# Performance work log

Measured on AMD Instinct MI355X. Metric: run time of the kernel, lower is better.

The kernel has to match this reference:

```python
import jax, jax.numpy as jnp
import numpy as np

B, N, D, C, IN, S = 64, 8192, 64, 256, 128, 3
CTRL_IN = IN + D  # input concatenated with 1 read vector
EPS = 1e-8


def _address(h, mem, prev_w, Wk, bk, Wb, bb, Wg, bg, Ws, bs, Wgam, bgam):
    """NTM content+location addressing. h:[B,C], mem:[B,N,D], prev_w:[B,N] -> [B,N]."""
    k = h @ Wk + bk                                   # [B,D]
    beta = jax.nn.softplus(h @ Wb + bb)               # [B,1]
    g = jax.nn.sigmoid(h @ Wg + bg)                   # [B,1]
    s = jax.nn.softmax(h @ Ws + bs, axis=-1)          # [B,S]
    gamma = jax.nn.softplus(h @ Wgam + bgam) + 1.0    # [B,1]
    # cosine similarity of key vs each memory row
    dots = jnp.einsum('bnd,bd->bn', mem, k)           # [B,N]
    norms = jnp.linalg.norm(mem, axis=-1) * jnp.linalg.norm(k, axis=-1, keepdims=True)
    sim = dots / (norms + EPS)
    wc = jax.nn.softmax(beta * sim, axis=-1)          # content weights
    wg = g * wc + (1.0 - g) * prev_w                  # interpolation gate
    # circular convolution with shift kernel, offsets [-1, 0, 1]
    offsets = [j - S // 2 for j in range(S)]
    ws = sum(s[:, j:j + 1] * jnp.roll(wg, offsets[j], axis=1) for j in range(S))
    # sharpening
    wpow = ws ** gamma
    return wpow / (jnp.sum(wpow, axis=-1, keepdims=True) + EPS)


def setup_inputs() -> dict:
    key = jax.random.key(0)
    ks = jax.random.split(key, 40)

    def p(k, shape):
        return jax.random.normal(k, shape, jnp.float32) / np.sqrt(shape[0]).astype(np.float32)

    inp = {
        'x': jax.random.normal(ks[0], (B, IN), jnp.float32),
        'prev_memory': jax.random.uniform(ks[1], (B, N, D), jnp.float32),
        'prev_read_weights': jax.random.uniform(ks[2], (B, N), jnp.float32),
        'prev_write_weights': jax.random.uniform(ks[3], (B, N), jnp.float32),
        'prev_read_vector': jax.random.normal(ks[4], (B, D), jnp.float32),
        # feedforward controller
        'W_ctrl': p(ks[5], (CTRL_IN, C)), 'b_ctrl': jnp.zeros((C,), jnp.float32),
        # read head
        'Wk_r': p(ks[6], (C, D)), 'bk_r': jnp.zeros((D,), jnp.float32),
        'Wb_r': p(ks[7], (C, 1)), 'bb_r': jnp.zeros((1,), jnp.float32),
        'Wg_r': p(ks[8], (C, 1)), 'bg_r': jnp.zeros((1,), jnp.float32),
        'Ws_r': p(ks[9], (C, S)), 'bs_r': jnp.zeros((S,), jnp.float32),
        'Wgam_r': p(ks[10], (C, 1)), 'bgam_r': jnp.zeros((1,), jnp.float32),
        # write head
        'Wk_w': p(ks[11], (C, D)), 'bk_w': jnp.zeros((D,), jnp.float32),
        'Wb_w': p(ks[12], (C, 1)), 'bb_w': jnp.zeros((1,), jnp.float32),
        'Wg_w': p(ks[13], (C, 1)), 'bg_w': jnp.zeros((1,), jnp.float32),
        'Ws_w': p(ks[14], (C, S)), 'bs_w': jnp.zeros((S,), jnp.float32),
        'Wgam_w': p(ks[15], (C, 1)), 'bgam_w': jnp.zeros((1,), jnp.float32),
        'We_w': p(ks[16], (C, D)), 'be_w': jnp.zeros((D,), jnp.float32),
        'Wa_w': p(ks[17], (C, D)), 'ba_w': jnp.zeros((D,), jnp.float32),
    }
    return inp


def reference(x, prev_memory, prev_read_weights, prev_write_weights, prev_read_vector,
              W_ctrl, b_ctrl,
              Wk_r, bk_r, Wb_r, bb_r, Wg_r, bg_r, Ws_r, bs_r, Wgam_r, bgam_r,
              Wk_w, bk_w, Wb_w, bb_w, Wg_w, bg_w, Ws_w, bs_w, Wgam_w, bgam_w,
              We_w, be_w, Wa_w, ba_w):
    # controller: Dense + relu over [input, prev read vector]
    ctrl_in = jnp.concatenate([x, prev_read_vector], axis=-1)    # [B, CTRL_IN]
    h = jax.nn.relu(ctrl_in @ W_ctrl + b_ctrl)                   # [B, C]

    # write head: addressing, then erase/add memory update
    w_w = _address(h, prev_memory, prev_write_weights,
                   Wk_w, bk_w, Wb_w, bb_w, Wg_w, bg_w, Ws_w, bs_w, Wgam_w, bgam_w)
    erase = jax.nn.sigmoid(h @ We_w + be_w)                      # [B, D]
    add = jnp.tanh(h @ Wa_w + ba_w)                              # [B, D]
    ww = w_w[:, :, None]                                         # [B, N, 1]
    new_memory = prev_memory * (1.0 - ww * erase[:, None, :]) + ww * add[:, None, :]

    # read head: addressing on updated memory, then weighted read
    w_r = _address(h, new_memory, prev_read_weights,
                   Wk_r, bk_r, Wb_r, bb_r, Wg_r, bg_r, Ws_r, bs_r, Wgam_r, bgam_r)
    read_vec = jnp.einsum('bnd,bn->bd', new_memory, w_r)         # [B, D]

    output = jnp.concatenate([h, read_vec], axis=-1)             # [B, C + D]
    return output
```

## Files before the change

### kernel.cpp

```cpp
#include <hip/hip_runtime.h>
#include <math.h>

#define Bb   64
#define Nn   8192
#define Dd   64
#define Cc   256
#define INn  128
#define CTRL 192
#define OUTW 320
#define EPSF 1e-8f
#define BN   (Bb*Nn)

#define OFF_P4 0
#define OFF_P2 (4*BN)
#define OFF_WW (6*BN)
#define OFF_WR (7*BN)
#define OFF_PT (8*BN)
#define OFF_BM (OFF_PT + 2048*64)
#define OFF_KW (OFF_BM + 2048)
#define OFF_KR (OFF_KW + Bb*Dd)
#define OFF_ER (OFF_KR + Bb*Dd)
#define OFF_AD (OFF_ER + Bb*Dd)
#define OFF_SC (OFF_AD + Bb*Dd)

__device__ __forceinline__ float softplusf(float x) {
    return (x > 20.f) ? x : log1pf(__expf(x));
}
__device__ __forceinline__ float sigmoidf(float x) {
    return 1.f / (1.f + __expf(-x));
}

__device__ __forceinline__ float blockSum1024(float v, float* red) {
    #pragma unroll
    for (int m = 32; m >= 1; m >>= 1) v += __shfl_xor(v, m);
    __syncthreads();
    if ((threadIdx.x & 63) == 0) red[threadIdx.x >> 6] = v;
    __syncthreads();
    float s = 0.f;
    #pragma unroll
    for (int i = 0; i < 16; ++i) s += red[i];
    return s;
}
__device__ __forceinline__ float blockMax1024(float v, float* red) {
    #pragma unroll
    for (int m = 32; m >= 1; m >>= 1) v = fmaxf(v, __shfl_xor(v, m));
    __syncthreads();
    if ((threadIdx.x & 63) == 0) red[threadIdx.x >> 6] = v;
    __syncthreads();
    float s = -1e30f;
    #pragma unroll
    for (int i = 0; i < 16; ++i) s = fmaxf(s, red[i]);
    return s;
}

struct SetupArgs {
    const float *x, *prv, *Wc, *bc;
    const float *Wk_r, *bk_r, *Wb_r, *bb_r, *Wg_r, *bg_r, *Ws_r, *bs_r, *Wgam_r, *bgam_r;
    const float *Wk_w, *bk_w, *Wb_w, *bb_w, *Wg_w, *bg_w, *Ws_w, *bs_w, *Wgam_w, *bgam_w;
    const float *We_w, *be_w, *Wa_w, *ba_w;
    float *ws, *out;
};

__global__ __launch_bounds__(256) void k_setup(SetupArgs a) {
    __shared__ float ci[CTRL];
    __shared__ float h[Cc];
    __shared__ alignas(16) float kbuf[128];
    __shared__ alignas(16) float abuf[64];
    __shared__ float red[4][16];
    __shared__ float sums[16];
    const int b = blockIdx.x, t = threadIdx.x;

    if (t < INn)       ci[t] = a.x[b * INn + t];
    else if (t < CTRL) ci[t] = a.prv[b * Dd + (t - INn)];
    __syncthreads();

    float acc = a.bc[t];
    #pragma unroll 16
    for (int i = 0; i < CTRL; ++i) acc += ci[i] * a.Wc[i * Cc + t];
    const float hv = fmaxf(acc, 0.f);
    h[t] = hv;
    a.out[b * OUTW + t] = hv;
    __syncthreads();

    {
        const int job = t >> 6, d = t & 63;
        const float* W  = (job == 0) ? a.Wk_w : (job == 1) ? a.Wk_r : (job == 2) ? a.We_w : a.Wa_w;
        const float* bs = (job == 0) ? a.bk_w : (job == 1) ? a.bk_r : (job == 2) ? a.be_w : a.ba_w;
        float p = bs[d];
        #pragma unroll 16
        for (int c = 0; c < Cc; ++c) p += h[c] * W[c * Dd + d];
        if (job == 0)      { a.ws[OFF_KW + b * Dd + d] = p; kbuf[d] = p; }
        else if (job == 1) { a.ws[OFF_KR + b * Dd + d] = p; kbuf[64 + d] = p; }
        else if (job == 2) { a.ws[OFF_ER + b * Dd + d] = sigmoidf(p); }
        else               { const float ad = tanhf(p); a.ws[OFF_AD + b * Dd + d] = ad; abuf[d] = ad; }
    }
    __syncthreads();

    float v[16];
    v[0] = hv * a.Wb_w[t];  v[1] = hv * a.Wg_w[t];  v[2] = hv * a.Wgam_w[t];
    v[3] = hv * a.Ws_w[t * 3 + 0]; v[4] = hv * a.Ws_w[t * 3 + 1]; v[5] = hv * a.Ws_w[t * 3 + 2];
    v[6] = hv * a.Wb_r[t];  v[7] = hv * a.Wg_r[t];  v[8] = hv * a.Wgam_r[t];
    v[9] = hv * a.Ws_r[t * 3 + 0]; v[10] = hv * a.Ws_r[t * 3 + 1]; v[11] = hv * a.Ws_r[t * 3 + 2];
    v[12] = (t < 64) ? kbuf[t] * kbuf[t] : 0.f;
    v[13] = (t >= 64 && t < 128) ? kbuf[t] * kbuf[t] : 0.f;
    v[14] = (t < 64) ? abuf[t] * kbuf[64 + t] : 0.f;
    v[15] = (t < 64) ? abuf[t] * abuf[t] : 0.f;
    #pragma unroll
    for (int k = 0; k < 16; ++k) {
        #pragma unroll
        for (int m = 32; m >= 1; m >>= 1) v[k] += __shfl_xor(v[k], m);
    }
    if ((t & 63) == 0) {
        #pragma unroll
        for (int k = 0; k < 16; ++k) red[t >> 6][k] = v[k];
    }
    __syncthreads();
    if (t < 16) sums[t] = red[0][t] + red[1][t] + red[2][t] + red[3][t];
    __syncthreads();

    if (t == 0) {
        float* sc = a.ws + OFF_SC + b * 16;
        sc[0] = softplusf(sums[0] + a.bb_w[0]);
        sc[1] = sigmoidf(sums[1] + a.bg_w[0]);
        sc[2] = softplusf(sums[2] + a.bgam_w[0]) + 1.f;
        sc[3] = sqrtf(sums[12]);
        sc[4] = softplusf(sums[6] + a.bb_r[0]);
        sc[5] = sigmoidf(sums[7] + a.bg_r[0]);
        sc[6] = softplusf(sums[8] + a.bgam_r[0]) + 1.f;
        sc[7] = sqrtf(sums[13]);
        {
            const float v0 = sums[3] + a.bs_w[0], v1 = sums[4] + a.bs_w[1], v2 = sums[5] + a.bs_w[2];
            const float m = fmaxf(fmaxf(v0, v1), v2);
            const float e0 = __expf(v0 - m), e1 = __expf(v1 - m), e2 = __expf(v2 - m);
            const float s = e0 + e1 + e2;
            sc[8] = e0 / s; sc[9] = e1 / s; sc[10] = e2 / s;
        }
        sc[11] = sums[14];
        {
            const float v0 = sums[9] + a.bs_r[0], v1 = sums[10] + a.bs_r[1], v2 = sums[11] + a.bs_r[2];
            const float m = fmaxf(fmaxf(v0, v1), v2);
            const float e0 = __expf(v0 - m), e1 = __expf(v1 - m), e2 = __expf(v2 - m);
            const float s = e0 + e1 + e2;
            sc[12] = e0 / s; sc[13] = e1 / s; sc[14] = e2 / s;
        }
        sc[15] = sums[15];
    }
}

__global__ __launch_bounds__(256) void k_pass1(const float* __restrict__ mem,
                                               float* __restrict__ ws) {
    __shared__ float redmax[4];
    const int t = threadIdx.x;
    const int wv = t >> 6, lane = t & 63;
    const int cg = lane & 7;
    const int rr = lane >> 3;
    const int wbase = blockIdx.x * 256 + wv * 64;
    const int b = wbase >> 13;
    const int cb = cg << 3;

    const float4 kwA = *(const float4*)(ws + OFF_KW + (b << 6) + cb);
    const float4 kwB = *(const float4*)(ws + OFF_KW + (b << 6) + cb + 4);
    const float4 krA = *(const float4*)(ws + OFF_KR + (b << 6) + cb);
    const float4 krB = *(const float4*)(ws + OFF_KR + (b << 6) + cb + 4);
    const float4 evA = *(const float4*)(ws + OFF_ER + (b << 6) + cb);
    const float4 evB = *(const float4*)(ws + OFF_ER + (b << 6) + cb + 4);
    const float4 avA = *(const float4*)(ws + OFF_AD + (b << 6) + cb);
    const float4 avB = *(const float4*)(ws + OFF_AD + (b << 6) + cb + 4);
    const float beta = ws[OFF_SC + b * 16 + 0];
    const float kn   = ws[OFF_SC + b * 16 + 3];

    float lmax = -1e30f;
    #pragma unroll 2
    for (int it = 0; it < 8; ++it) {
        const int row = wbase + (it << 3) + rr;
        const float* mp = mem + ((size_t)row << 6) + cb;
        const float4 m0 = *(const float4*)(mp);
        const float4 m1 = *(const float4*)(mp + 4);
        float dw = 0.f, dr = 0.f, nq = 0.f, e1 = 0.f, e2 = 0.f, c5 = 0.f;
        #define ACC(mv, kwv, krv, evv, avv) { \
            const float me = (mv) * (evv); \
            dw = fmaf((mv), (kwv), dw); \
            dr = fmaf((mv), (krv), dr); \
            nq = fmaf((mv), (mv), nq); \
            e1 = fmaf((mv), (avv) - me, e1); \
            e2 = fmaf(me, fmaf(-2.f, (avv), me), e2); \
            c5 = fmaf(me, (krv), c5); }
        ACC(m0.x, kwA.x, krA.x, evA.x, avA.x)
        ACC(m0.y, kwA.y, krA.y, evA.y, avA.y)
        ACC(m0.z, kwA.z, krA.z, evA.z, avA.z)
        ACC(m0.w, kwA.w, krA.w, evA.w, avA.w)
        ACC(m1.x, kwB.x, krB.x, evB.x, avB.x)
        ACC(m1.y, kwB.y, krB.y, evB.y, avB.y)
        ACC(m1.z, kwB.z, krB.z, evB.z, avB.z)
        ACC(m1.w, kwB.w, krB.w, evB.w, avB.w)
        #undef ACC
        #pragma unroll
        for (int mk = 1; mk <= 4; mk <<= 1) {
            dw += __shfl_xor(dw, mk); dr += __shfl_xor(dr, mk);
            nq += __shfl_xor(nq, mk); e1 += __shfl_xor(e1, mk);
            e2 += __shfl_xor(e2, mk); c5 += __shfl_xor(c5, mk);
        }
        const float xw = beta * dw / (sqrtf(nq) * kn + EPSF);
        lmax = fmaxf(lmax, xw);
        if (cg == 0) {
            float4 p4; p4.x = xw; p4.y = dr; p4.z = c5; p4.w = nq;
            *(float4*)(ws + OFF_P4 + ((size_t)row << 2)) = p4;
            float2 p2; p2.x = e1; p2.y = e2;
            *(float2*)(ws + OFF_P2 + ((size_t)row << 1)) = p2;
        }
    }
    lmax = fmaxf(lmax, __shfl_xor(lmax, 8));
    lmax = fmaxf(lmax, __shfl_xor(lmax, 16));
    lmax = fmaxf(lmax, __shfl_xor(lmax, 32));
    if (lane == 0) redmax[wv] = lmax;
    __syncthreads();
    if (t == 0)
        ws[OFF_BM + blockIdx.x] = fmaxf(fmaxf(redmax[0], redmax[1]),
                                        fmaxf(redmax[2], redmax[3]));
}

__global__ __launch_bounds__(1024, 4) void k_addrBoth(float* __restrict__ ws,
                                                      const float* __restrict__ prevw_w,
                                                      const float* __restrict__ prevw_r) {
    __shared__ float buf[Nn];
    __shared__ float red[16];
    const int b = blockIdx.x, t = threadIdx.x;
    const int bN = b * Nn;
    const int base = t << 3;
    const float* sc = ws + OFF_SC + b * 16;
    const float g_w = sc[1], gam_w = sc[2];
    const float s0w = sc[8], s1w = sc[9], s2w = sc[10];
    const float beta_r = sc[4], g_r = sc[5], gam_r = sc[6], kn_r = sc[7];
    const float AK = sc[11], A2 = sc[15];
    const float s0r = sc[12], s1r = sc[13], s2r = sc[14];

    float M = -1e30f;
    #pragma unroll
    for (int i = 0; i < 32; ++i) M = fmaxf(M, ws[OFF_BM + b * 32 + i]);

    float4 p4[8]; float2 p2[8];
    #pragma unroll
    for (int i = 0; i < 8; ++i) p4[i] = *(const float4*)(ws + OFF_P4 + ((size_t)(bN + base + i) << 2));
    #pragma unroll
    for (int i = 0; i < 8; ++i) p2[i] = *(const float2*)(ws + OFF_P2 + ((size_t)(bN + base + i) << 1));
    const float4 pw0 = *(const float4*)(prevw_w + bN + base);
    const float4 pw1 = *(const float4*)(prevw_w + bN + base + 4);
    const float4 pr0 = *(const float4*)(prevw_r + bN + base);
    const float4 pr1 = *(const float4*)(prevw_r + bN + base + 4);

    float xs[8];
    float pw[8] = {pw0.x, pw0.y, pw0.z, pw0.w, pw1.x, pw1.y, pw1.z, pw1.w};
    float lsum = 0.f;
    #pragma unroll
    for (int i = 0; i < 8; ++i) { const float e = __expf(p4[i].x - M); xs[i] = e; lsum += e; }
    const float S = blockSum1024(lsum, red);
    const float sinv = 1.f / S;
    #pragma unroll
    for (int i = 0; i < 8; ++i) buf[base + i] = g_w * xs[i] * sinv + (1.f - g_w) * pw[i];
    __syncthreads();
    {
        float nb[10];
        nb[0] = buf[(base + Nn - 1) & (Nn - 1)];
        #pragma unroll
        for (int i = 0; i < 8; ++i) nb[i + 1] = buf[base + i];
        nb[9] = buf[(base + 8) & (Nn - 1)];
        float lps = 0.f;
        #pragma unroll
        for (int i = 0; i < 8; ++i) {
            const float wsv = s0w * nb[i + 2] + s1w * nb[i + 1] + s2w * nb[i];
            const float wp = __expf(gam_w * __logf(wsv));
            xs[i] = wp; lps += wp;
        }
        const float PS = blockSum1024(lps, red);
        const float pinv = 1.f / (PS + EPSF);
        #pragma unroll
        for (int i = 0; i < 8; ++i) xs[i] *= pinv;
    }
    {
        float4 w0, w1;
        w0.x = xs[0]; w0.y = xs[1]; w0.z = xs[2]; w0.w = xs[3];
        w1.x = xs[4]; w1.y = xs[5]; w1.z = xs[6]; w1.w = xs[7];
        *(float4*)(ws + OFF_WW + bN + base) = w0;
        *(float4*)(ws + OFF_WW + bN + base + 4) = w1;
    }

    float lmax = -1e30f;
    #pragma unroll
    for (int i = 0; i < 8; ++i) {
        const float w = xs[i];
        const float d = p4[i].y + w * (AK - p4[i].z);
        float qq = p4[i].w + 2.f * w * p2[i].x + w * w * (p2[i].y + A2);
        qq = fmaxf(qq, 0.f);
        const float x = beta_r * d / (sqrtf(qq) * kn_r + EPSF);
        xs[i] = x; lmax = fmaxf(lmax, x);
    }
    const float Mr = blockMax1024(lmax, red);
    float lsr = 0.f;
    #pragma unroll
    for (int i = 0; i < 8; ++i) { const float e = __expf(xs[i] - Mr); xs[i] = e; lsr += e; }
    const float Sr = blockSum1024(lsr, red);
    const float srinv = 1.f / Sr;
    float prv[8] = {pr0.x, pr0.y, pr0.z, pr0.w, pr1.x, pr1.y, pr1.z, pr1.w};
    __syncthreads();
    #pragma unroll
    for (int i = 0; i < 8; ++i) buf[base + i] = g_r * xs[i] * srinv + (1.f - g_r) * prv[i];
    __syncthreads();
    {
        float nb[10];
        nb[0] = buf[(base + Nn - 1) & (Nn - 1)];
        #pragma unroll
        for (int i = 0; i < 8; ++i) nb[i + 1] = buf[base + i];
        nb[9] = buf[(base + 8) & (Nn - 1)];
        float lpr = 0.f;
        #pragma unroll
        for (int i = 0; i < 8; ++i) {
            const float wsv = s0r * nb[i + 2] + s1r * nb[i + 1] + s2r * nb[i];
            const float wp = __expf(gam_r * __logf(wsv));
            xs[i] = wp; lpr += wp;
        }
        const float PSr = blockSum1024(lpr, red);
        const float prinv = 1.f / (PSr + EPSF);
        float4 w0, w1;
        w0.x = xs[0] * prinv; w0.y = xs[1] * prinv; w0.z = xs[2] * prinv; w0.w = xs[3] * prinv;
        w1.x = xs[4] * prinv; w1.y = xs[5] * prinv; w1.z = xs[6] * prinv; w1.w = xs[7] * prinv;
        *(float4*)(ws + OFF_WR + bN + base) = w0;
        *(float4*)(ws + OFF_WR + bN + base + 4) = w1;
    }
}

__global__ __launch_bounds__(256) void k_read(const float* __restrict__ mem,
                                              float* __restrict__ ws) {
    __shared__ float lds[4 * 64];
    const int b = blockIdx.x >> 5;
    const int chunk = blockIdx.x & 31;
    const int t = threadIdx.x;
    const int lane = t & 63, wv = t >> 6;
    const int q = lane & 15, r = lane >> 4;
    const float4 evv = *(const float4*)(ws + OFF_ER + (b << 6) + (q << 2));
    const float4 avv = *(const float4*)(ws + OFF_AD + (b << 6) + (q << 2));
    float a0 = 0.f, a1 = 0.f, a2 = 0.f, a3 = 0.f;
    const int base_n = chunk << 8;
    #pragma unroll 4
    for (int gi = wv; gi < 64; gi += 4) {
        const int n = base_n + (gi << 2) + r;
        const int row = b * Nn + n;
        const float4 mv = *(const float4*)(mem + ((size_t)row << 6) + (q << 2));
        const float w   = ws[OFF_WW + row];
        const float wrv = ws[OFF_WR + row];
        a0 = fmaf((mv.x * (1.f - w * evv.x) + w * avv.x), wrv, a0);
        a1 = fmaf((mv.y * (1.f - w * evv.y) + w * avv.y), wrv, a1);
        a2 = fmaf((mv.z * (1.f - w * evv.z) + w * avv.z), wrv, a2);
        a3 = fmaf((mv.w * (1.f - w * evv.w) + w * avv.w), wrv, a3);
    }
    #pragma unroll
    for (int m = 16; m <= 32; m <<= 1) {
        a0 += __shfl_xor(a0, m); a1 += __shfl_xor(a1, m);
        a2 += __shfl_xor(a2, m); a3 += __shfl_xor(a3, m);
    }
    if (r == 0) {
        lds[wv * 64 + q * 4 + 0] = a0; lds[wv * 64 + q * 4 + 1] = a1;
        lds[wv * 64 + q * 4 + 2] = a2; lds[wv * 64 + q * 4 + 3] = a3;
    }
    __syncthreads();
    if (t < 64) {
        ws[OFF_PT + blockIdx.x * 64 + t] = lds[t] + lds[64 + t] + lds[128 + t] + lds[192 + t];
    }
}

__global__ __launch_bounds__(64) void k_reduce(const float* __restrict__ ws,
                                               float* __restrict__ out) {
    const int b = blockIdx.x, d = threadIdx.x;
    float s = 0.f;
    #pragma unroll
    for (int i = 0; i < 32; ++i) s += ws[OFF_PT + ((b << 5) + i) * 64 + d];
    out[b * OUTW + 256 + d] = s;
}

extern "C" void kernel_launch(void* const* d_in, const int* in_sizes, int n_in,
                              void* d_out, int out_size, void* d_ws, size_t ws_size,
                              hipStream_t stream) {
    const float* x      = (const float*)d_in[0];
    const float* mem    = (const float*)d_in[1];
    const float* prw_r  = (const float*)d_in[2];
    const float* prw_w  = (const float*)d_in[3];
    const float* prv    = (const float*)d_in[4];

    float* ws  = (float*)d_ws;
    float* out = (float*)d_out;

    SetupArgs a;
    a.x = x; a.prv = prv;
    a.Wc = (const float*)d_in[5];  a.bc = (const float*)d_in[6];
    a.Wk_r = (const float*)d_in[7];  a.bk_r = (const float*)d_in[8];
    a.Wb_r = (const float*)d_in[9];  a.bb_r = (const float*)d_in[10];
    a.Wg_r = (const float*)d_in[11]; a.bg_r = (const float*)d_in[12];
    a.Ws_r = (const float*)d_in[13]; a.bs_r = (const float*)d_in[14];
    a.Wgam_r = (const float*)d_in[15]; a.bgam_r = (const float*)d_in[16];
    a.Wk_w = (const float*)d_in[17]; a.bk_w = (const float*)d_in[18];
    a.Wb_w = (const float*)d_in[19]; a.bb_w = (const float*)d_in[20];
    a.Wg_w = (const float*)d_in[21]; a.bg_w = (const float*)d_in[22];
    a.Ws_w = (const float*)d_in[23]; a.bs_w = (const float*)d_in[24];
    a.Wgam_w = (const float*)d_in[25]; a.bgam_w = (const float*)d_in[26];
    a.We_w = (const float*)d_in[27]; a.be_w = (const float*)d_in[28];
    a.Wa_w = (const float*)d_in[29]; a.ba_w = (const float*)d_in[30];
    a.ws = ws; a.out = out;

    k_setup<<<Bb, 256, 0, stream>>>(a);
    k_pass1<<<2048, 256, 0, stream>>>(mem, ws);
    k_addrBoth<<<Bb, 1024, 0, stream>>>(ws, prw_w, prw_r);
    k_read<<<Bb * 32, 256, 0, stream>>>(mem, ws);
    k_reduce<<<Bb, 64, 0, stream>>>(ws, out);
}
```

Before: 89.16 us.

## Split per-batch addressing kernel into grid-wide kernels with online-softmax partials

Replaces the 64-block addressing kernel, which had one 1024-thread block per batch, with three 2048-block kernels (write side, read similarity, read finalize). Each chunk does its own halo-based circular shift and writes partial max/sum or sum values. Pass1 now folds an online max+sum softmax into its loop, so the write softmax needs no separate sum pass. Final normalization is deferred into the consumers (k_rside, k_read). The aim is to fill the GPU instead of running 64 large serialized blocks, at the cost of extra launches and extra workspace traffic.

```diff
diff --git a/kernel.cpp b/kernel.cpp
--- a/kernel.cpp
+++ b/kernel.cpp
@@ -11,17 +11,20 @@
 #define EPSF 1e-8f
 #define BN   (Bb*Nn)
 
-#define OFF_P4 0
-#define OFF_P2 (4*BN)
-#define OFF_WW (6*BN)
-#define OFF_WR (7*BN)
-#define OFF_PT (8*BN)
-#define OFF_BM (OFF_PT + 2048*64)
-#define OFF_KW (OFF_BM + 2048)
-#define OFF_KR (OFF_KW + Bb*Dd)
-#define OFF_ER (OFF_KR + Bb*Dd)
-#define OFF_AD (OFF_ER + Bb*Dd)
-#define OFF_SC (OFF_AD + Bb*Dd)
+#define OFF_P4  0
+#define OFF_P2  (4*BN)
+#define OFF_WPW (6*BN)
+#define OFF_WPR (7*BN)
+#define OFF_PT  (8*BN)
+#define OFF_MS  (OFF_PT + 2048*64)
+#define OFF_PW  (OFF_MS + 4096)
+#define OFF_MSR (OFF_PW + 2048)
+#define OFF_PR  (OFF_MSR + 4096)
+#define OFF_KW  (OFF_PR + 2048)
+#define OFF_KR  (OFF_KW + Bb*Dd)
+#define OFF_ER  (OFF_KR + Bb*Dd)
+#define OFF_AD  (OFF_ER + Bb*Dd)
+#define OFF_SC  (OFF_AD + Bb*Dd)
 
 __device__ __forceinline__ float softplusf(float x) {
     return (x > 20.f) ? x : log1pf(__expf(x));
@@ -29,28 +32,10 @@
 __device__ __forceinline__ float sigmoidf(float x) {
     return 1.f / (1.f + __expf(-x));
 }
-
-__device__ __forceinline__ float blockSum1024(float v, float* red) {
-    #pragma unroll
-    for (int m = 32; m >= 1; m >>= 1) v += __shfl_xor(v, m);
-    __syncthreads();
-    if ((threadIdx.x & 63) == 0) red[threadIdx.x >> 6] = v;
-    __syncthreads();
-    float s = 0.f;
-    #pragma unroll
-    for (int i = 0; i < 16; ++i) s += red[i];
-    return s;
-}
-__device__ __forceinline__ float blockMax1024(float v, float* red) {
-    #pragma unroll
-    for (int m = 32; m >= 1; m >>= 1) v = fmaxf(v, __shfl_xor(v, m));
-    __syncthreads();
-    if ((threadIdx.x & 63) == 0) red[threadIdx.x >> 6] = v;
-    __syncthreads();
-    float s = -1e30f;
-    #pragma unroll
-    for (int i = 0; i < 16; ++i) s = fmaxf(s, red[i]);
-    return s;
+__device__ __forceinline__ void msCombine(float& m, float& s, float m2, float s2) {
+    const float mn = fmaxf(m, m2);
+    s = s * __expf(m - mn) + s2 * __expf(m2 - mn);
+    m = mn;
 }
 
 struct SetupArgs {
@@ -149,7 +134,7 @@
 
 __global__ __launch_bounds__(256) void k_pass1(const float* __restrict__ mem,
                                                float* __restrict__ ws) {
-    __shared__ float redmax[4];
+    __shared__ float redm[4], reds[4];
     const int t = threadIdx.x;
     const int wv = t >> 6, lane = t & 63;
     const int cg = lane & 7;
@@ -169,7 +154,7 @@
     const float beta = ws[OFF_SC + b * 16 + 0];
     const float kn   = ws[OFF_SC + b * 16 + 3];
 
-    float lmax = -1e30f;
+    float om = -1e30f, os = 0.f;
     #pragma unroll 2
     for (int it = 0; it < 8; ++it) {
         const int row = wbase + (it << 3) + rr;
@@ -201,7 +186,8 @@
             e2 += __shfl_xor(e2, mk); c5 += __shfl_xor(c5, mk);
         }
         const float xw = beta * dw / (sqrtf(nq) * kn + EPSF);
-        lmax = fmaxf(lmax, xw);
+        if (xw > om) { os = os * __expf(om - xw) + 1.f; om = xw; }
+        else         { os += __expf(xw - om); }
         if (cg == 0) {
             float4 p4; p4.x = xw; p4.y = dr; p4.z = c5; p4.w = nq;
             *(float4*)(ws + OFF_P4 + ((size_t)row << 2)) = p4;
@@ -209,133 +195,190 @@
             *(float2*)(ws + OFF_P2 + ((size_t)row << 1)) = p2;
         }
     }
-    lmax = fmaxf(lmax, __shfl_xor(lmax, 8));
-    lmax = fmaxf(lmax, __shfl_xor(lmax, 16));
-    lmax = fmaxf(lmax, __shfl_xor(lmax, 32));
-    if (lane == 0) redmax[wv] = lmax;
-    __syncthreads();
-    if (t == 0)
-        ws[OFF_BM + blockIdx.x] = fmaxf(fmaxf(redmax[0], redmax[1]),
-                                        fmaxf(redmax[2], redmax[3]));
-}
-
-__global__ __launch_bounds__(1024, 4) void k_addrBoth(float* __restrict__ ws,
-                                                      const float* __restrict__ prevw_w,
-                                                      const float* __restrict__ prevw_r) {
-    __shared__ float buf[Nn];
-    __shared__ float red[16];
-    const int b = blockIdx.x, t = threadIdx.x;
+    #pragma unroll
+    for (int mk = 1; mk <= 32; mk <<= 1) {
+        const float m2 = __shfl_xor(om, mk), s2 = __shfl_xor(os, mk);
+        msCombine(om, os, m2, s2);
+    }
+    if (lane == 0) { redm[wv] = om; reds[wv] = os; }
+    __syncthreads();
+    if (t == 0) {
+        float M = redm[0], S = reds[0];
+        msCombine(M, S, redm[1], reds[1]);
+        msCombine(M, S, redm[2], reds[2]);
+        msCombine(M, S, redm[3], reds[3]);
+        ws[OFF_MS + (blockIdx.x << 1)]     = M;
+        ws[OFF_MS + (blockIdx.x << 1) + 1] = S * 0.125f;
+    }
+}
+
+__global__ __launch_bounds__(256) void k_wside(const float* __restrict__ prevw_w,
+                                               float* __restrict__ ws) {
+    __shared__ float wgbuf[258];
+    __shared__ float red[6];
+    const int blk = blockIdx.x, t = threadIdx.x;
+    const int b = blk >> 5;
+    const int rbl = (blk & 31) << 8;
     const int bN = b * Nn;
-    const int base = t << 3;
+
+    if (t < 64) {
+        float m = -1e30f, s = 0.f;
+        if (t < 32) {
+            m = ws[OFF_MS + (((b << 5) + t) << 1)];
+            s = ws[OFF_MS + (((b << 5) + t) << 1) + 1];
+        }
+        #pragma unroll
+        for (int mk = 1; mk <= 32; mk <<= 1) {
+            const float m2 = __shfl_xor(m, mk), s2 = __shfl_xor(s, mk);
+            msCombine(m, s, m2, s2);
+        }
+        if (t == 0) { red[4] = m; red[5] = 1.f / s; }
+    }
+    __syncthreads();
+    const float M = red[4], invS = red[5];
     const float* sc = ws + OFF_SC + b * 16;
-    const float g_w = sc[1], gam_w = sc[2];
-    const float s0w = sc[8], s1w = sc[9], s2w = sc[10];
-    const float beta_r = sc[4], g_r = sc[5], gam_r = sc[6], kn_r = sc[7];
-    const float AK = sc[11], A2 = sc[15];
-    const float s0r = sc[12], s1r = sc[13], s2r = sc[14];
-
-    float M = -1e30f;
-    #pragma unroll
-    for (int i = 0; i < 32; ++i) M = fmaxf(M, ws[OFF_BM + b * 32 + i]);
-
-    float4 p4[8]; float2 p2[8];
-    #pragma unroll
-    for (int i = 0; i < 8; ++i) p4[i] = *(const float4*)(ws + OFF_P4 + ((size_t)(bN + base + i) << 2));
-    #pragma unroll
-    for (int i = 0; i < 8; ++i) p2[i] = *(const float2*)(ws + OFF_P2 + ((size_t)(bN + base + i) << 1));
-    const float4 pw0 = *(const float4*)(prevw_w + bN + base);
-    const float4 pw1 = *(const float4*)(prevw_w + bN + base + 4);
-    const float4 pr0 = *(const float4*)(prevw_r + bN + base);
-    const float4 pr1 = *(const float4*)(prevw_r + bN + base + 4);
-
-    float xs[8];
-    float pw[8] = {pw0.x, pw0.y, pw0.z, pw0.w, pw1.x, pw1.y, pw1.z, pw1.w};
-    float lsum = 0.f;
-    #pragma unroll
-    for (int i = 0; i < 8; ++i) { const float e = __expf(p4[i].x - M); xs[i] = e; lsum += e; }
-    const float S = blockSum1024(lsum, red);
-    const float sinv = 1.f / S;
-    #pragma unroll
-    for (int i = 0; i < 8; ++i) buf[base + i] = g_w * xs[i] * sinv + (1.f - g_w) * pw[i];
-    __syncthreads();
-    {
-        float nb[10];
-        nb[0] = buf[(base + Nn - 1) & (Nn - 1)];
-        #pragma unroll
-        for (int i = 0; i < 8; ++i) nb[i + 1] = buf[base + i];
-        nb[9] = buf[(base + 8) & (Nn - 1)];
-        float lps = 0.f;
-        #pragma unroll
-        for (int i = 0; i < 8; ++i) {
-            const float wsv = s0w * nb[i + 2] + s1w * nb[i + 1] + s2w * nb[i];
-            const float wp = __expf(gam_w * __logf(wsv));
-            xs[i] = wp; lps += wp;
-        }
-        const float PS = blockSum1024(lps, red);
-        const float pinv = 1.f / (PS + EPSF);
-        #pragma unroll
-        for (int i = 0; i < 8; ++i) xs[i] *= pinv;
-    }
-    {
-        float4 w0, w1;
-        w0.x = xs[0]; w0.y = xs[1]; w0.z = xs[2]; w0.w = xs[3];
-        w1.x = xs[4]; w1.y = xs[5]; w1.z = xs[6]; w1.w = xs[7];
-        *(float4*)(ws + OFF_WW + bN + base) = w0;
-        *(float4*)(ws + OFF_WW + bN + base + 4) = w1;
-    }
-
-    float lmax = -1e30f;
-    #pragma unroll
-    for (int i = 0; i < 8; ++i) {
-        const float w = xs[i];
-        const float d = p4[i].y + w * (AK - p4[i].z);
-        float qq = p4[i].w + 2.f * w * p2[i].x + w * w * (p2[i].y + A2);
-        qq = fmaxf(qq, 0.f);
-        const float x = beta_r * d / (sqrtf(qq) * kn_r + EPSF);
-        xs[i] = x; lmax = fmaxf(lmax, x);
-    }
-    const float Mr = blockMax1024(lmax, red);
-    float lsr = 0.f;
-    #pragma unroll
-    for (int i = 0; i < 8; ++i) { const float e = __expf(xs[i] - Mr); xs[i] = e; lsr += e; }
-    const float Sr = blockSum1024(lsr, red);
-    const float srinv = 1.f / Sr;
-    float prv[8] = {pr0.x, pr0.y, pr0.z, pr0.w, pr1.x, pr1.y, pr1.z, pr1.w};
-    __syncthreads();
-    #pragma unroll
-    for (int i = 0; i < 8; ++i) buf[base + i] = g_r * xs[i] * srinv + (1.f - g_r) * prv[i];
-    __syncthreads();
-    {
-        float nb[10];
-        nb[0] = buf[(base + Nn - 1) & (Nn - 1)];
-        #pragma unroll
-        for (int i = 0; i < 8; ++i) nb[i + 1] = buf[base + i];
-        nb[9] = buf[(base + 8) & (Nn - 1)];
-        float lpr = 0.f;
-        #pragma unroll
-        for (int i = 0; i < 8; ++i) {
-            const float wsv = s0r * nb[i + 2] + s1r * nb[i + 1] + s2r * nb[i];
-            const float wp = __expf(gam_r * __logf(wsv));
-            xs[i] = wp; lpr += wp;
-        }
-        const float PSr = blockSum1024(lpr, red);
-        const float prinv = 1.f / (PSr + EPSF);
-        float4 w0, w1;
-        w0.x = xs[0] * prinv; w0.y = xs[1] * prinv; w0.z = xs[2] * prinv; w0.w = xs[3] * prinv;
-        w1.x = xs[4] * prinv; w1.y = xs[5] * prinv; w1.z = xs[6] * prinv; w1.w = xs[7] * prinv;
-        *(float4*)(ws + OFF_WR + bN + base) = w0;
-        *(float4*)(ws + OFF_WR + bN + base + 4) = w1;
-    }
+    const float g = sc[1], gam = sc[2];
+    const float s0 = sc[8], s1 = sc[9], s2 = sc[10];
+
+    auto wg_at = [&](int i) {
+        const int rg = bN + ((rbl + i - 1) & (Nn - 1));
+        const float xw = ws[OFF_P4 + ((size_t)rg << 2)];
+        return g * __expf(xw - M) * invS + (1.f - g) * prevw_w[rg];
+    };
+    wgbuf[t + 1] = wg_at(t + 1);
+    if (t == 0)   wgbuf[0]   = wg_at(0);
+    if (t == 255) wgbuf[257] = wg_at(257);
+    __syncthreads();
+
+    const float wsv = s0 * wgbuf[t + 2] + s1 * wgbuf[t + 1] + s2 * wgbuf[t];
+    const float wp = __expf(gam * __logf(wsv));
+    ws[OFF_WPW + bN + rbl + t] = wp;
+
+    float v = wp;
+    #pragma unroll
+    for (int mk = 1; mk <= 32; mk <<= 1) v += __shfl_xor(v, mk);
+    if ((t & 63) == 0) red[t >> 6] = v;
+    __syncthreads();
+    if (t == 0) ws[OFF_PW + blk] = red[0] + red[1] + red[2] + red[3];
+}
+
+__global__ __launch_bounds__(256) void k_rside(float* __restrict__ ws) {
+    __shared__ float redm[4], reds[4];
+    __shared__ float inv[1];
+    const int blk = blockIdx.x, t = threadIdx.x;
+    const int b = blk >> 5;
+    const int rbl = (blk & 31) << 8;
+    const int bN = b * Nn;
+
+    if (t < 64) {
+        float v = (t < 32) ? ws[OFF_PW + (b << 5) + t] : 0.f;
+        #pragma unroll
+        for (int mk = 1; mk <= 32; mk <<= 1) v += __shfl_xor(v, mk);
+        if (t == 0) inv[0] = 1.f / (v + EPSF);
+    }
+    __syncthreads();
+    const float invW = inv[0];
+    const float* sc = ws + OFF_SC + b * 16;
+    const float beta_r = sc[4], kn_r = sc[7], AK = sc[11], A2 = sc[15];
+
+    const int row = bN + rbl + t;
+    const float ww = ws[OFF_WPW + row] * invW;
+    const float4 p4 = *(const float4*)(ws + OFF_P4 + ((size_t)row << 2));
+    const float2 p2 = *(const float2*)(ws + OFF_P2 + ((size_t)row << 1));
+    const float d = p4.y + ww * (AK - p4.z);
+    float qq = p4.w + 2.f * ww * p2.x + ww * ww * (p2.y + A2);
+    qq = fmaxf(qq, 0.f);
+    const float x = beta_r * d / (sqrtf(qq) * kn_r + EPSF);
+    ws[OFF_P2 + ((size_t)row << 1)] = x;
+
+    float om = x, os = 1.f;
+    #pragma unroll
+    for (int mk = 1; mk <= 32; mk <<= 1) {
+        const float m2 = __shfl_xor(om, mk), s2 = __shfl_xor(os, mk);
+        msCombine(om, os, m2, s2);
+    }
+    if ((t & 63) == 0) { redm[t >> 6] = om; reds[t >> 6] = os; }
+    __syncthreads();
+    if (t == 0) {
+        float M = redm[0], S = reds[0];
+        msCombine(M, S, redm[1], reds[1]);
+        msCombine(M, S, redm[2], reds[2]);
+        msCombine(M, S, redm[3], reds[3]);
+        ws[OFF_MSR + (blk << 1)]     = M;
+        ws[OFF_MSR + (blk << 1) + 1] = S;
+    }
+}
+
+__global__ __launch_bounds__(256) void k_rfin(const float* __restrict__ prevw_r,
+                                              float* __restrict__ ws) {
+    __shared__ float wgbuf[258];
+    __shared__ float red[6];
+    const int blk = blockIdx.x, t = threadIdx.x;
+    const int b = blk >> 5;
+    const int rbl = (blk & 31) << 8;
+    const int bN = b * Nn;
+
+    if (t < 64) {
+        float m = -1e30f, s = 0.f;
+        if (t < 32) {
+            m = ws[OFF_MSR + (((b << 5) + t) << 1)];
+            s = ws[OFF_MSR + (((b << 5) + t) << 1) + 1];
+        }
+        #pragma unroll
+        for (int mk = 1; mk <= 32; mk <<= 1) {
+            const float m2 = __shfl_xor(m, mk), s2 = __shfl_xor(s, mk);
+            msCombine(m, s, m2, s2);
+        }
+        if (t == 0) { red[4] = m; red[5] = 1.f / s; }
+    }
+    __syncthreads();
+    const float M = red[4], invS = red[5];
+    const float* sc = ws + OFF_SC + b * 16;
+    const float g = sc[5], gam = sc[6];
+    const float s0 = sc[12], s1 = sc[13], s2 = sc[14];
+
+    auto wg_at = [&](int i) {
+        const int rg = bN + ((rbl + i - 1) & (Nn - 1));
+        const float xr = ws[OFF_P2 + ((size_t)rg << 1)];
+        return g * __expf(xr - M) * invS + (1.f - g) * prevw_r[rg];
+    };
+    wgbuf[t + 1] = wg_at(t + 1);
+    if (t == 0)   wgbuf[0]   = wg_at(0);
+    if (t == 255) wgbuf[257] = wg_at(257);
+    __syncthreads();
+
+    const float wsv = s0 * wgbuf[t + 2] + s1 * wgbuf[t + 1] + s2 * wgbuf[t];
+    const float wp = __expf(gam * __logf(wsv));
+    ws[OFF_WPR + bN + rbl + t] = wp;
+
+    float v = wp;
+    #pragma unroll
+    for (int mk = 1; mk <= 32; mk <<= 1) v += __shfl_xor(v, mk);
+    if ((t & 63) == 0) red[t >> 6] = v;
+    __syncthreads();
+    if (t == 0) ws[OFF_PR + blk] = red[0] + red[1] + red[2] + red[3];
 }
 
 __global__ __launch_bounds__(256) void k_read(const float* __restrict__ mem,
                                               float* __restrict__ ws) {
     __shared__ float lds[4 * 64];
+    __shared__ float invb[2];
     const int b = blockIdx.x >> 5;
     const int chunk = blockIdx.x & 31;
     const int t = threadIdx.x;
     const int lane = t & 63, wv = t >> 6;
     const int q = lane & 15, r = lane >> 4;
+
+    if (t < 64) {
+        float vw = (t < 32) ? ws[OFF_PW + (b << 5) + t] : 0.f;
+        float vr = (t < 32) ? ws[OFF_PR + (b << 5) + t] : 0.f;
+        #pragma unroll
+        for (int mk = 1; mk <= 32; mk <<= 1) { vw += __shfl_xor(vw, mk); vr += __shfl_xor(vr, mk); }
+        if (t == 0) { invb[0] = 1.f / (vw + EPSF); invb[1] = 1.f / (vr + EPSF); }
+    }
+    __syncthreads();
+    const float invW = invb[0], invR = invb[1];
+
     const float4 evv = *(const float4*)(ws + OFF_ER + (b << 6) + (q << 2));
     const float4 avv = *(const float4*)(ws + OFF_AD + (b << 6) + (q << 2));
     float a0 = 0.f, a1 = 0.f, a2 = 0.f, a3 = 0.f;
@@ -345,8 +388,8 @@
         const int n = base_n + (gi << 2) + r;
         const int row = b * Nn + n;
         const float4 mv = *(const float4*)(mem + ((size_t)row << 6) + (q << 2));
-        const float w   = ws[OFF_WW + row];
-        const float wrv = ws[OFF_WR + row];
+        const float w   = ws[OFF_WPW + row] * invW;
+        const float wrv = ws[OFF_WPR + row] * invR;
         a0 = fmaf((mv.x * (1.f - w * evv.x) + w * avv.x), wrv, a0);
         a1 = fmaf((mv.y * (1.f - w * evv.y) + w * avv.y), wrv, a1);
         a2 = fmaf((mv.z * (1.f - w * evv.z) + w * avv.z), wrv, a2);
@@ -405,9 +448,11 @@
     a.Wa_w = (const float*)d_in[29]; a.ba_w = (const float*)d_in[30];
     a.ws = ws; a.out = out;
 
-    k_setup<<<Bb, 256, 0, stream>>>(a);
-    k_pass1<<<2048, 256, 0, stream>>>(mem, ws);
-    k_addrBoth<<<Bb, 1024, 0, stream>>>(ws, prw_w, prw_r);
-    k_read<<<Bb * 32, 256, 0, stream>>>(mem, ws);
-    k_reduce<<<Bb, 64, 0, stream>>>(ws, out);
-}
+    k_setup <<<Bb,   256, 0, stream>>>(a);
+    k_pass1 <<<2048, 256, 0, stream>>>(mem, ws);
+    k_wside <<<2048, 256, 0, stream>>>(prw_w, ws);
+    k_rside <<<2048, 256, 0, stream>>>(ws);
+    k_rfin  <<<2048, 256, 0, stream>>>(prw_r, ws);
+    k_read  <<<2048, 256, 0, stream>>>(mem, ws);
+    k_reduce<<<Bb,   64,  0, stream>>>(ws, out);
+}
```

Measured after the change: 90.52 us. About the same (+1.5%).

## Compute online softmax partials in pass1 and transpose reductions through LDS

Applied to the files above, without the earlier changes.

The memory pass now handles 32 rows per wave and reduces the per-row partial sums with an LDS transpose instead of three rounds of shuffles over six values. It also emits per-block online-softmax (max, sum) pairs, so the addressing kernel skips one block-wide exp-sum reduction and merges 64 pairs instead. The workspace is relaid out so the write logits sit in a contiguous array and the remaining per-row partials are packed as float4 plus a separate scalar, which gives more vectorised loads. The cost is more LDS per block, an extra block barrier, extra exp work for the combine steps, and twice as many pass1 blocks.

```diff
diff --git a/kernel.cpp b/kernel.cpp
--- a/kernel.cpp
+++ b/kernel.cpp
@@ -11,23 +11,29 @@
 #define EPSF 1e-8f
 #define BN   (Bb*Nn)
 
-#define OFF_P4 0
-#define OFF_P2 (4*BN)
-#define OFF_WW (6*BN)
-#define OFF_WR (7*BN)
-#define OFF_PT (8*BN)
-#define OFF_BM (OFF_PT + 2048*64)
-#define OFF_KW (OFF_BM + 2048)
-#define OFF_KR (OFF_KW + Bb*Dd)
-#define OFF_ER (OFF_KR + Bb*Dd)
-#define OFF_AD (OFF_ER + Bb*Dd)
-#define OFF_SC (OFF_AD + Bb*Dd)
+#define OFF_XW  0
+#define OFF_P4  BN
+#define OFF_E2  (5*BN)
+#define OFF_WPW (6*BN)
+#define OFF_WPR (7*BN)
+#define OFF_PT  (8*BN)
+#define OFF_MS  (OFF_PT + 131072)
+#define OFF_KW  (OFF_MS + 8192)
+#define OFF_KR  (OFF_KW + Bb*Dd)
+#define OFF_ER  (OFF_KR + Bb*Dd)
+#define OFF_AD  (OFF_ER + Bb*Dd)
+#define OFF_SC  (OFF_AD + Bb*Dd)
 
 __device__ __forceinline__ float softplusf(float x) {
     return (x > 20.f) ? x : log1pf(__expf(x));
 }
 __device__ __forceinline__ float sigmoidf(float x) {
     return 1.f / (1.f + __expf(-x));
+}
+__device__ __forceinline__ void msCombine(float& m, float& s, float m2, float s2) {
+    const float mn = fmaxf(m, m2);
+    s = s * __expf(m - mn) + s2 * __expf(m2 - mn);
+    m = mn;
 }
 
 __device__ __forceinline__ float blockSum1024(float v, float* red) {
@@ -149,13 +155,15 @@
 
 __global__ __launch_bounds__(256) void k_pass1(const float* __restrict__ mem,
                                                float* __restrict__ ws) {
-    __shared__ float redmax[4];
+    __shared__ float tr[4][32 * 49];
+    __shared__ float wm[4], wsum[4];
     const int t = threadIdx.x;
     const int wv = t >> 6, lane = t & 63;
     const int cg = lane & 7;
     const int rr = lane >> 3;
-    const int wbase = blockIdx.x * 256 + wv * 64;
-    const int b = wbase >> 13;
+    const int tile = (blockIdx.x << 2) + wv;
+    const int rowbase = tile << 5;
+    const int b = rowbase >> 13;
     const int cb = cg << 3;
 
     const float4 kwA = *(const float4*)(ws + OFF_KW + (b << 6) + cb);
@@ -169,10 +177,10 @@
     const float beta = ws[OFF_SC + b * 16 + 0];
     const float kn   = ws[OFF_SC + b * 16 + 3];
 
-    float lmax = -1e30f;
-    #pragma unroll 2
-    for (int it = 0; it < 8; ++it) {
-        const int row = wbase + (it << 3) + rr;
+    float acc[4][6];
+    #pragma unroll
+    for (int s = 0; s < 4; ++s) {
+        const int row = rowbase + (s << 3) + rr;
         const float* mp = mem + ((size_t)row << 6) + cb;
         const float4 m0 = *(const float4*)(mp);
         const float4 m1 = *(const float4*)(mp + 4);
@@ -194,29 +202,56 @@
         ACC(m1.z, kwB.z, krB.z, evB.z, avB.z)
         ACC(m1.w, kwB.w, krB.w, evB.w, avB.w)
         #undef ACC
-        #pragma unroll
-        for (int mk = 1; mk <= 4; mk <<= 1) {
-            dw += __shfl_xor(dw, mk); dr += __shfl_xor(dr, mk);
-            nq += __shfl_xor(nq, mk); e1 += __shfl_xor(e1, mk);
-            e2 += __shfl_xor(e2, mk); c5 += __shfl_xor(c5, mk);
-        }
-        const float xw = beta * dw / (sqrtf(nq) * kn + EPSF);
-        lmax = fmaxf(lmax, xw);
-        if (cg == 0) {
-            float4 p4; p4.x = xw; p4.y = dr; p4.z = c5; p4.w = nq;
-            *(float4*)(ws + OFF_P4 + ((size_t)row << 2)) = p4;
-            float2 p2; p2.x = e1; p2.y = e2;
-            *(float2*)(ws + OFF_P2 + ((size_t)row << 1)) = p2;
-        }
-    }
-    lmax = fmaxf(lmax, __shfl_xor(lmax, 8));
-    lmax = fmaxf(lmax, __shfl_xor(lmax, 16));
-    lmax = fmaxf(lmax, __shfl_xor(lmax, 32));
-    if (lane == 0) redmax[wv] = lmax;
-    __syncthreads();
-    if (t == 0)
-        ws[OFF_BM + blockIdx.x] = fmaxf(fmaxf(redmax[0], redmax[1]),
-                                        fmaxf(redmax[2], redmax[3]));
+        acc[s][0] = dw; acc[s][1] = dr; acc[s][2] = nq;
+        acc[s][3] = e1; acc[s][4] = e2; acc[s][5] = c5;
+    }
+
+    float* T = tr[wv];
+    #pragma unroll
+    for (int s = 0; s < 4; ++s) {
+        #pragma unroll
+        for (int v = 0; v < 6; ++v)
+            T[((s << 3) + rr) * 49 + cg * 6 + v] = acc[s][v];
+    }
+    __syncthreads();
+
+    const int rd = lane & 31;
+    const int gb = (lane >> 5) << 2;
+    float dw = 0.f, dr = 0.f, nq = 0.f, e1 = 0.f, e2 = 0.f, c5 = 0.f;
+    #pragma unroll
+    for (int g = 0; g < 4; ++g) {
+        const float* p = T + rd * 49 + (gb + g) * 6;
+        dw += p[0]; dr += p[1]; nq += p[2];
+        e1 += p[3]; e2 += p[4]; c5 += p[5];
+    }
+    dw += __shfl_xor(dw, 32); dr += __shfl_xor(dr, 32); nq += __shfl_xor(nq, 32);
+    e1 += __shfl_xor(e1, 32); e2 += __shfl_xor(e2, 32); c5 += __shfl_xor(c5, 32);
+
+    const int row = rowbase + rd;
+    const float xw = beta * dw / (sqrtf(nq) * kn + EPSF);
+    if (lane < 32) {
+        ws[OFF_XW + row] = xw;
+        float4 p4; p4.x = dr; p4.y = c5; p4.z = nq; p4.w = e1;
+        *(float4*)(ws + OFF_P4 + ((size_t)row << 2)) = p4;
+        ws[OFF_E2 + row] = e2;
+    }
+
+    float om = xw, os = 1.f;
+    #pragma unroll
+    for (int mk = 1; mk <= 32; mk <<= 1) {
+        const float m2 = __shfl_xor(om, mk), s2 = __shfl_xor(os, mk);
+        msCombine(om, os, m2, s2);
+    }
+    if (lane == 0) { wm[wv] = om; wsum[wv] = os; }
+    __syncthreads();
+    if (t == 0) {
+        float M = wm[0], S = wsum[0];
+        msCombine(M, S, wm[1], wsum[1]);
+        msCombine(M, S, wm[2], wsum[2]);
+        msCombine(M, S, wm[3], wsum[3]);
+        ws[OFF_MS + (blockIdx.x << 1)]     = M;
+        ws[OFF_MS + (blockIdx.x << 1) + 1] = S * 0.5f;
+    }
 }
 
 __global__ __launch_bounds__(1024, 4) void k_addrBoth(float* __restrict__ ws,
@@ -224,6 +259,7 @@
                                                       const float* __restrict__ prevw_r) {
     __shared__ float buf[Nn];
     __shared__ float red[16];
+    __shared__ float sMS[2];
     const int b = blockIdx.x, t = threadIdx.x;
     const int bN = b * Nn;
     const int base = t << 3;
@@ -234,29 +270,37 @@
     const float AK = sc[11], A2 = sc[15];
     const float s0r = sc[12], s1r = sc[13], s2r = sc[14];
 
-    float M = -1e30f;
-    #pragma unroll
-    for (int i = 0; i < 32; ++i) M = fmaxf(M, ws[OFF_BM + b * 32 + i]);
-
-    float4 p4[8]; float2 p2[8];
-    #pragma unroll
-    for (int i = 0; i < 8; ++i) p4[i] = *(const float4*)(ws + OFF_P4 + ((size_t)(bN + base + i) << 2));
-    #pragma unroll
-    for (int i = 0; i < 8; ++i) p2[i] = *(const float2*)(ws + OFF_P2 + ((size_t)(bN + base + i) << 1));
+    if (t < 64) {
+        float m = ws[OFF_MS + ((b * 64 + t) << 1)];
+        float s = ws[OFF_MS + ((b * 64 + t) << 1) + 1];
+        #pragma unroll
+        for (int mk = 1; mk <= 32; mk <<= 1) {
+            const float m2 = __shfl_xor(m, mk), s2 = __shfl_xor(s, mk);
+            msCombine(m, s, m2, s2);
+        }
+        if (t == 0) { sMS[0] = m; sMS[1] = 1.f / s; }
+    }
+
+    const float4 xw0 = *(const float4*)(ws + OFF_XW + bN + base);
+    const float4 xw1 = *(const float4*)(ws + OFF_XW + bN + base + 4);
     const float4 pw0 = *(const float4*)(prevw_w + bN + base);
     const float4 pw1 = *(const float4*)(prevw_w + bN + base + 4);
+    float4 p4[8];
+    #pragma unroll
+    for (int i = 0; i < 8; ++i)
+        p4[i] = *(const float4*)(ws + OFF_P4 + ((size_t)(bN + base + i) << 2));
+    const float4 e20 = *(const float4*)(ws + OFF_E2 + bN + base);
+    const float4 e21 = *(const float4*)(ws + OFF_E2 + bN + base + 4);
     const float4 pr0 = *(const float4*)(prevw_r + bN + base);
     const float4 pr1 = *(const float4*)(prevw_r + bN + base + 4);
-
-    float xs[8];
+    __syncthreads();
+    const float M = sMS[0], invS = sMS[1];
+
+    float xs[8] = {xw0.x, xw0.y, xw0.z, xw0.w, xw1.x, xw1.y, xw1.z, xw1.w};
     float pw[8] = {pw0.x, pw0.y, pw0.z, pw0.w, pw1.x, pw1.y, pw1.z, pw1.w};
-    float lsum = 0.f;
-    #pragma unroll
-    for (int i = 0; i < 8; ++i) { const float e = __expf(p4[i].x - M); xs[i] = e; lsum += e; }
-    const float S = blockSum1024(lsum, red);
-    const float sinv = 1.f / S;
-    #pragma unroll
-    for (int i = 0; i < 8; ++i) buf[base + i] = g_w * xs[i] * sinv + (1.f - g_w) * pw[i];
+    #pragma unroll
+    for (int i = 0; i < 8; ++i)
+        buf[base + i] = g_w * __expf(xs[i] - M) * invS + (1.f - g_w) * pw[i];
     __syncthreads();
     {
         float nb[10];
@@ -280,16 +324,17 @@
         float4 w0, w1;
         w0.x = xs[0]; w0.y = xs[1]; w0.z = xs[2]; w0.w = xs[3];
         w1.x = xs[4]; w1.y = xs[5]; w1.z = xs[6]; w1.w = xs[7];
-        *(float4*)(ws + OFF_WW + bN + base) = w0;
-        *(float4*)(ws + OFF_WW + bN + base + 4) = w1;
-    }
-
+        *(float4*)(ws + OFF_WPW + bN + base) = w0;
+        *(float4*)(ws + OFF_WPW + bN + base + 4) = w1;
+    }
+
+    const float e2a[8] = {e20.x, e20.y, e20.z, e20.w, e21.x, e21.y, e21.z, e21.w};
     float lmax = -1e30f;
     #pragma unroll
     for (int i = 0; i < 8; ++i) {
         const float w = xs[i];
-        const float d = p4[i].y + w * (AK - p4[i].z);
-        float qq = p4[i].w + 2.f * w * p2[i].x + w * w * (p2[i].y + A2);
+        const float d = p4[i].x + w * (AK - p4[i].y);
+        float qq = p4[i].z + 2.f * w * p4[i].w + w * w * (e2a[i] + A2);
         qq = fmaxf(qq, 0.f);
         const float x = beta_r * d / (sqrtf(qq) * kn_r + EPSF);
         xs[i] = x; lmax = fmaxf(lmax, x);
@@ -300,10 +345,11 @@
     for (int i = 0; i < 8; ++i) { const float e = __expf(xs[i] - Mr); xs[i] = e; lsr += e; }
     const float Sr = blockSum1024(lsr, red);
     const float srinv = 1.f / Sr;
-    float prv[8] = {pr0.x, pr0.y, pr0.z, pr0.w, pr1.x, pr1.y, pr1.z, pr1.w};
-    __syncthreads();
-    #pragma unroll
-    for (int i = 0; i < 8; ++i) buf[base + i] = g_r * xs[i] * srinv + (1.f - g_r) * prv[i];
+    const float prv8[8] = {pr0.x, pr0.y, pr0.z, pr0.w, pr1.x, pr1.y, pr1.z, pr1.w};
+    __syncthreads();
+    #pragma unroll
+    for (int i = 0; i < 8; ++i)
+        buf[base + i] = g_r * xs[i] * srinv + (1.f - g_r) * prv8[i];
     __syncthreads();
     {
         float nb[10];
@@ -323,8 +369,8 @@
         float4 w0, w1;
         w0.x = xs[0] * prinv; w0.y = xs[1] * prinv; w0.z = xs[2] * prinv; w0.w = xs[3] * prinv;
         w1.x = xs[4] * prinv; w1.y = xs[5] * prinv; w1.z = xs[6] * prinv; w1.w = xs[7] * prinv;
-        *(float4*)(ws + OFF_WR + bN + base) = w0;
-        *(float4*)(ws + OFF_WR + bN + base + 4) = w1;
+        *(float4*)(ws + OFF_WPR + bN + base) = w0;
+        *(float4*)(ws + OFF_WPR + bN + base + 4) = w1;
     }
 }
 
@@ -336,6 +382,7 @@
     const int t = threadIdx.x;
     const int lane = t & 63, wv = t >> 6;
     const int q = lane & 15, r = lane >> 4;
+
     const float4 evv = *(const float4*)(ws + OFF_ER + (b << 6) + (q << 2));
     const float4 avv = *(const float4*)(ws + OFF_AD + (b << 6) + (q << 2));
     float a0 = 0.f, a1 = 0.f, a2 = 0.f, a3 = 0.f;
@@ -345,8 +392,8 @@
         const int n = base_n + (gi << 2) + r;
         const int row = b * Nn + n;
         const float4 mv = *(const float4*)(mem + ((size_t)row << 6) + (q << 2));
-        const float w   = ws[OFF_WW + row];
-        const float wrv = ws[OFF_WR + row];
+        const float w   = ws[OFF_WPW + row];
+        const float wrv = ws[OFF_WPR + row];
         a0 = fmaf((mv.x * (1.f - w * evv.x) + w * avv.x), wrv, a0);
         a1 = fmaf((mv.y * (1.f - w * evv.y) + w * avv.y), wrv, a1);
         a2 = fmaf((mv.z * (1.f - w * evv.z) + w * avv.z), wrv, a2);
@@ -405,9 +452,9 @@
     a.Wa_w = (const float*)d_in[29]; a.ba_w = (const float*)d_in[30];
     a.ws = ws; a.out = out;
 
-    k_setup<<<Bb, 256, 0, stream>>>(a);
-    k_pass1<<<2048, 256, 0, stream>>>(mem, ws);
-    k_addrBoth<<<Bb, 1024, 0, stream>>>(ws, prw_w, prw_r);
-    k_read<<<Bb * 32, 256, 0, stream>>>(mem, ws);
-    k_reduce<<<Bb, 64, 0, stream>>>(ws, out);
-}
+    k_setup   <<<Bb,   256,  0, stream>>>(a);
+    k_pass1   <<<4096, 256,  0, stream>>>(mem, ws);
+    k_addrBoth<<<Bb,   1024, 0, stream>>>(ws, prw_w, prw_r);
+    k_read    <<<2048, 256,  0, stream>>>(mem, ws);
+    k_reduce  <<<Bb,   64,   0, stream>>>(ws, out);
+}
```

Measured after the change: 82.23 us, median of 2. 7.8% less time.
